# Kernel tuning notes

Hardware: AMD Instinct MI355X
Metric: run time of the kernel (lower is better)

The kernel has to match this reference:

```python
import jax, jax.numpy as jnp
import numpy as np

N = 50000   # nodes per node type
D = 256     # in_dim == out_dim
H = 8       # num heads
DK = D // H # 32
E = 500000  # edges per edge type
LN_EPS = 1e-5


def setup_inputs() -> dict:
    key = jax.random.key(0)
    ks = jax.random.split(key, 16)
    w = lambda k, shape: jax.random.normal(k, shape, dtype=jnp.float32) * 0.05
    xav = np.sqrt(6.0 / (DK + DK))
    return {
        'feats': jax.random.normal(ks[0], (2, N, D), dtype=jnp.float32),
        'Wk': w(ks[1], (2, D, D)), 'bk': jnp.zeros((2, D), jnp.float32),
        'Wq': w(ks[2], (2, D, D)), 'bq': jnp.zeros((2, D), jnp.float32),
        'Wv': w(ks[3], (2, D, D)), 'bv': jnp.zeros((2, D), jnp.float32),
        'Wa': w(ks[4], (2, D, D)), 'ba': jnp.zeros((2, D), jnp.float32),
        'ln_w': jnp.ones((2, D), jnp.float32), 'ln_b': jnp.zeros((2, D), jnp.float32),
        'skip': jnp.ones((2,), jnp.float32),
        'mu': jnp.ones((2, H), jnp.float32),
        'w_att': jax.random.uniform(ks[5], (2, H, DK, DK), jnp.float32, -xav, xav),
        'w_msg': jax.random.uniform(ks[6], (2, H, DK, DK), jnp.float32, -xav, xav),
        'src': jax.random.randint(ks[7], (2, E), 0, N, dtype=jnp.int32),
        'dst': jax.random.randint(ks[8], (2, E), 0, N, dtype=jnp.int32),
    }


def _edge_softmax(scores, seg, n):
    # scores: (E, H); softmax over edges sharing the same destination node
    m = jax.ops.segment_max(scores, seg, num_segments=n)          # (N, H)
    e = jnp.exp(scores - m[seg])
    s = jax.ops.segment_sum(e, seg, num_segments=n)               # (N, H)
    return e / s[seg]


def _forward(feats, Wk, bk, Wq, bq, Wv, bv, Wa, ba, ln_w, ln_b, skip,
             mu, w_att, w_msg, src, dst):
    # canonical etypes: 0 = author->paper, 1 = paper->author
    stypes, dtypes = (0, 1), (1, 0)
    scale = 1.0 / jnp.sqrt(jnp.asarray(DK, feats.dtype))
    h = [None, None]
    for et in range(2):
        st, dt = stypes[et], dtypes[et]
        s_idx, d_idx = src[et], dst[et]
        k = (feats[st] @ Wk[st] + bk[st]).reshape(N, H, DK)
        k = jnp.einsum('nhi,hij->nhj', k, w_att[et])
        v = (feats[st] @ Wv[st] + bv[st]).reshape(N, H, DK)
        v = jnp.einsum('nhi,hij->nhj', v, w_msg[et])
        q = (feats[dt] @ Wq[dt] + bq[dt]).reshape(N, H, DK)
        t = jnp.einsum('ehd,ehd->eh', q[d_idx], k[s_idx])         # (E, H)
        attn = _edge_softmax(t * mu[et] * scale, d_idx, N)        # (E, H)
        msg = v[s_idx] * attn[..., None]                          # (E, H, DK)
        h[dt] = jax.ops.segment_sum(msg, d_idx, num_segments=N).reshape(N, D)
    h = jnp.stack(h)  # (2, N, D); each ntype receives from exactly one etype

    trans = jnp.einsum('tnd,tde->tne', h, Wa) + ba[:, None, :]
    alpha = jax.nn.sigmoid(skip)[:, None, None]
    out = alpha * trans + (1.0 - alpha) * feats
    mean = out.mean(-1, keepdims=True)
    var = out.var(-1, keepdims=True)
    out = (out - mean) * jax.lax.rsqrt(var + LN_EPS)
    return out * ln_w[:, None, :] + ln_b[:, None, :]


def reference(feats, Wk, bk, Wq, bq, Wv, bv, Wa, ba, ln_w, ln_b, skip,
              mu, w_att, w_msg, src, dst):
    return _forward(feats, Wk, bk, Wq, bq, Wv, bv, Wa, ba, ln_w, ln_b, skip,
                    mu, w_att, w_msg, src, dst)
```

## Files before the change

### kernel.cpp

```cpp
#include <hip/hip_runtime.h>
#include <hip/hip_bf16.h>

#define D 256
#define H 8
#define DK 32

typedef unsigned short ushort_t;
typedef unsigned int uint_t;
typedef __attribute__((ext_vector_type(4))) float floatx4;
typedef __attribute__((ext_vector_type(2))) float floatx2;
typedef __attribute__((ext_vector_type(8))) short shortx8;
typedef __attribute__((ext_vector_type(8))) unsigned short ushortx8;

typedef __attribute__((address_space(3))) void lds_void_t;
typedef const __attribute__((address_space(1))) void gbl_void_t;

__device__ __forceinline__ float b2f(ushort_t u) {
    return __uint_as_float(((uint_t)u) << 16);
}
__device__ __forceinline__ floatx2 b2x2(uint_t u) {
    floatx2 r;
    r.x = __uint_as_float(u << 16);
    r.y = __uint_as_float(u & 0xffff0000u);
    return r;
}
__device__ __forceinline__ ushort_t f2b(float f) {
    uint_t u = __float_as_uint(f);
    uint_t r = (u + 0x7FFFu + ((u >> 16) & 1u)) >> 16;
    return (ushort_t)r;
}
__device__ __forceinline__ void async_cp16(const void* g, void* l) {
    __builtin_amdgcn_global_load_lds((gbl_void_t*)g, (lds_void_t*)l, 16, 0, 0);
}

__global__ void cvt_bf16(const float* __restrict__ in, ushort_t* __restrict__ out, size_t n4) {
    size_t i = (size_t)blockIdx.x * blockDim.x + threadIdx.x;
    if (i >= n4) return;
    float4 v = ((const float4*)in)[i];
    ushort4 o;
    o.x = f2b(v.x); o.y = f2b(v.y); o.z = f2b(v.z); o.w = f2b(v.w);
    ((ushort4*)out)[i] = o;
}

__global__ void zero_int(int* __restrict__ p, int n) {
    int i = blockIdx.x * blockDim.x + threadIdx.x;
    if (i < n) p[i] = 0;
}

__global__ void fold_weights(const float* __restrict__ Wk, const float* __restrict__ bk,
                             const float* __restrict__ Wv, const float* __restrict__ bv,
                             const float* __restrict__ w_att, const float* __restrict__ w_msg,
                             float* __restrict__ Wkc, float* __restrict__ bkc,
                             float* __restrict__ Wvc, float* __restrict__ bvc) {
    int r = blockIdx.x, et = blockIdx.y, which = blockIdx.z;
    int tid = threadIdx.x;
    const float* Wsrc = (which ? Wv : Wk) + (size_t)et * D * D + (size_t)r * D;
    const float* wt   = (which ? w_msg : w_att) + (size_t)et * H * DK * DK;
    float* Wdst = (which ? Wvc : Wkc) + (size_t)et * D * D;
    __shared__ float wrow[D];
    wrow[tid] = Wsrc[tid];
    __syncthreads();
    int h = tid >> 5, j = tid & 31;
    const float* wth = wt + h * DK * DK;
    float acc = 0.f;
#pragma unroll 8
    for (int i = 0; i < DK; i++) acc += wrow[h * 32 + i] * wth[i * 32 + j];
    Wdst[(size_t)r * D + tid] = acc;
    if (r == 0) {
        const float* bsrc = (which ? bv : bk) + et * D;
        float* bdst = (which ? bvc : bkc) + et * D;
        float bacc = 0.f;
#pragma unroll 8
        for (int i = 0; i < DK; i++) bacc += bsrc[h * 32 + i] * wth[i * 32 + j];
        bdst[tid] = bacc;
    }
}

__global__ void pack_weights(const float* __restrict__ Wq, const float* __restrict__ bq,
                             const float* __restrict__ Wkc, const float* __restrict__ bkc,
                             const float* __restrict__ Wvc, const float* __restrict__ bvc,
                             const float* __restrict__ Wa,
                             ushort_t* __restrict__ WT_all, ushort_t* __restrict__ WaT,
                             float* __restrict__ bias_all) {
    int idx = blockIdx.x * blockDim.x + threadIdx.x;
    const int NW = 2 * 768 * 256;
    if (idx < NW) {
        int t = idx / (768 * 256);
        int rem = idx - t * 768 * 256;
        int n = rem >> 8, k = rem & 255;
        int sec = n >> 8, nn = n & 255;
        const float* W = (sec == 0) ? Wq : (sec == 1) ? Wkc : Wvc;
        WT_all[idx] = f2b(W[(size_t)t * D * D + (size_t)k * D + nn]);
    } else if (idx < NW + 2 * 256 * 256) {
        int r = idx - NW;
        int t = r / (256 * 256);
        int rem = r - t * 256 * 256;
        int n = rem >> 8, k = rem & 255;
        WaT[r] = f2b(Wa[(size_t)t * D * D + (size_t)k * D + n]);
    }
    if (idx < 2 * 768) {
        int t = idx / 768, n = idx % 768;
        int sec = n >> 8, nn = n & 255;
        const float* b = (sec == 0) ? bq : (sec == 1) ? bkc : bvc;
        bias_all[idx] = b[t * D + nn];
    }
}

#define TM 128
#define TN 128
#define TKK 32
__launch_bounds__(256)
__global__ void gemm_mfma(const ushort_t* __restrict__ A0, int lda, size_t aStr,
                          const ushort_t* __restrict__ BT0, size_t bStr,
                          const float* __restrict__ bias0, int biasStr,
                          ushort_t* __restrict__ C0, int ldc, size_t cStr,
                          int cShift, int M) {
    __shared__ ushort_t As[2][TM * TKK];
    __shared__ ushort_t Bs[2][TN * TKK];
    int tid = threadIdx.x;
    int w = tid >> 6, lane = tid & 63;
    int t = blockIdx.z;
    const ushort_t* A  = A0 + (size_t)t * aStr;
    const ushort_t* BT = BT0 + (size_t)t * bStr;
    const float* bias  = bias0 + (size_t)t * biasStr;
    ushort_t* C        = C0 + (size_t)t * cStr;

    int nwg  = gridDim.x * gridDim.y;
    int orig = blockIdx.y * gridDim.x + blockIdx.x;
    int q = nwg >> 3, r = nwg & 7;
    int xcd = orig & 7, loc = orig >> 3;
    int wgid = (xcd < r ? xcd * (q + 1) : r * (q + 1) + (xcd - r) * q) + loc;
    int ncol = gridDim.y;
    int rowt = wgid / ncol;
    int colt = wgid - rowt * ncol;
    int bm = rowt * TM;
    int bn = colt * TN;

    int wm = (w & 1) * 64, wn = (w >> 1) * 64;

    floatx4 acc[4][4] = {};

    int srow = lane >> 2;
    int scol = (lane & 3) * 8;
    int fr = lane & 15, fq = lane >> 4;

#define GEMM_STAGE(b, kc)                                                     \
    {                                                                         \
        _Pragma("unroll")                                                     \
        for (int j = 0; j < 2; j++) {                                         \
            int rr = w * 32 + j * 16;                                         \
            int gr = bm + rr + srow; if (gr >= M) gr = M - 1;                 \
            async_cp16(A + (size_t)gr * lda + (kc) + scol, As[b] + rr * TKK); \
            int gn = bn + rr + srow;                                          \
            async_cp16(BT + (size_t)gn * 256 + (kc) + scol, Bs[b] + rr * TKK);\
        }                                                                     \
    }

    GEMM_STAGE(0, 0);
#pragma unroll
    for (int s = 0; s < 8; s++) {
        int cur = s & 1;
        if (s < 7) {
            GEMM_STAGE(cur ^ 1, (s + 1) * TKK);
            __builtin_amdgcn_s_waitcnt(0x0F74);
        } else {
            __builtin_amdgcn_s_waitcnt(0x0F70);
        }
        __syncthreads();

        shortx8 af[4], bf[4];
#pragma unroll
        for (int i = 0; i < 4; i++)
            af[i] = *(const shortx8*)(As[cur] + (wm + i * 16 + fr) * TKK + fq * 8);
#pragma unroll
        for (int j = 0; j < 4; j++)
            bf[j] = *(const shortx8*)(Bs[cur] + (wn + j * 16 + fr) * TKK + fq * 8);
#pragma unroll
        for (int i = 0; i < 4; i++)
#pragma unroll
            for (int j = 0; j < 4; j++)
                acc[i][j] = __builtin_amdgcn_mfma_f32_16x16x32_bf16(af[i], bf[j], acc[i][j], 0, 0, 0);
        __syncthreads();
    }
#undef GEMM_STAGE

#pragma unroll
    for (int i = 0; i < 4; i++) {
#pragma unroll
        for (int j = 0; j < 4; j++) {
            int col = bn + wn + j * 16 + fr;
            float bv = bias[col];
#pragma unroll
            for (int rr = 0; rr < 4; rr++) {
                int row = bm + wm + i * 16 + fq * 4 + rr;
                if (row < M) C[(size_t)row * ldc + cShift + col] = f2b(acc[i][j][rr] + bv);
            }
        }
    }
}

__global__ void count_deg(const int* __restrict__ dst, int* __restrict__ deg,
                          int N, int E) {
    int i = blockIdx.x * blockDim.x + threadIdx.x;
    if (i >= 2 * E) return;
    int et = i / E, e = i - et * E;
    int d = dst[(size_t)et * E + e];
    atomicAdd(&deg[(1 - et) * N + d], 1);
}

__launch_bounds__(256)
__global__ void scan_blocks(int* __restrict__ deg, int* __restrict__ bsum, int n) {
    __shared__ int wsum[4];
    int tid = threadIdx.x, lane = tid & 63, w = tid >> 6;
    int i = blockIdx.x * 256 + tid;
    int v = (i < n) ? deg[i] : 0;
    int x = v;
#pragma unroll
    for (int off = 1; off < 64; off <<= 1) {
        int y = __shfl_up(x, off);
        if (lane >= off) x += y;
    }
    if (lane == 63) wsum[w] = x;
    __syncthreads();
    int add = 0;
    if (w > 0) add += wsum[0];
    if (w > 1) add += wsum[1];
    if (w > 2) add += wsum[2];
    int incl = x + add;
    if (i < n) deg[i] = incl - v;
    if (tid == 255) bsum[blockIdx.x] = incl;
}

__launch_bounds__(512)
__global__ void scan_tops(int* __restrict__ bsum, int* __restrict__ row_ptr,
                          int nb, int n) {
    __shared__ int wsum[8];
    int tid = threadIdx.x, lane = tid & 63, w = tid >> 6;
    int v = (tid < nb) ? bsum[tid] : 0;
    int x = v;
#pragma unroll
    for (int off = 1; off < 64; off <<= 1) {
        int y = __shfl_up(x, off);
        if (lane >= off) x += y;
    }
    if (lane == 63) wsum[w] = x;
    __syncthreads();
    int add = 0;
    for (int j = 0; j < w; j++) add += wsum[j];
    int incl = x + add;
    if (tid < nb) bsum[tid] = incl - v;
    if (tid == nb - 1) row_ptr[n] = incl;
}

__launch_bounds__(256)
__global__ void scan_apply(const int* __restrict__ excl, const int* __restrict__ bsum,
                           int* __restrict__ row_ptr, int* __restrict__ cursor, int n) {
    int i = blockIdx.x * 256 + threadIdx.x;
    if (i >= n) return;
    int e = excl[i] + bsum[blockIdx.x];
    row_ptr[i] = e;
    cursor[i] = e;
}

__global__ void fill_edges(const int* __restrict__ src, const int* __restrict__ dst,
                           int* __restrict__ cursor, int* __restrict__ ebuf,
                           int N, int E) {
    int i = blockIdx.x * blockDim.x + threadIdx.x;
    if (i >= 2 * E) return;
    int et = i / E, e = i - et * E;
    int d = dst[(size_t)et * E + e];
    int s = src[(size_t)et * E + e];
    int pos = atomicAdd(&cursor[(1 - et) * N + d], 1);
    ebuf[pos] = s;
}

__launch_bounds__(256)
__global__ void node_aggregate(ushort_t* __restrict__ QKV, const float* __restrict__ mu,
                               const int* __restrict__ row_ptr, const int* __restrict__ ebuf,
                               int N) {
    int wid = (blockIdx.x * blockDim.x + threadIdx.x) >> 6;
    int lane = threadIdx.x & 63;
    if (wid >= 2 * N) return;
    int dt = (wid >= N) ? 1 : 0;
    int et = 1 - dt;
    int l = lane & 31;
    int half = lane >> 5;
    int h = l >> 2;

    uint4 qu = ((const uint4*)(QKV + (size_t)wid * 768))[l];
    floatx2 q01 = b2x2(qu.x), q23 = b2x2(qu.y), q45 = b2x2(qu.z), q67 = b2x2(qu.w);
    float sc = mu[et * H + h] * 0.17677669529663687f;
    int beg = row_ptr[wid], end = row_ptr[wid + 1];
    const ushort_t* KVb = QKV + (size_t)et * N * 768 + l * 8;

    floatx2 a01 = {0.f, 0.f}, a23 = {0.f, 0.f}, a45 = {0.f, 0.f}, a67 = {0.f, 0.f};
    float ssum = 0.f;

#define AGG_COMPUTE(kk, vv)                                              \
    {                                                                    \
        floatx2 pv = q01 * b2x2(kk.x);                                   \
        pv += q23 * b2x2(kk.y);                                          \
        pv += q45 * b2x2(kk.z);                                          \
        pv += q67 * b2x2(kk.w);                                          \
        float pp = pv.x + pv.y;                                          \
        pp += __shfl_xor(pp, 1);                                         \
        pp += __shfl_xor(pp, 2);                                         \
        float ex = __expf(pp * sc);                                      \
        ssum += ex;                                                      \
        floatx2 e2 = {ex, ex};                                           \
        a01 += e2 * b2x2(vv.x);                                          \
        a23 += e2 * b2x2(vv.y);                                          \
        a45 += e2 * b2x2(vv.z);                                          \
        a67 += e2 * b2x2(vv.w);                                          \
    }

    int p = beg + half;
    uint4 kA = {}, vA = {}, kB = {}, vB = {};
    int sC = 0, sD = 0;
    if (p < end) {
        int sA = ebuf[p];
        const ushort_t* r0 = KVb + (size_t)sA * 768;
        kA = *(const uint4*)(r0 + 256);
        vA = *(const uint4*)(r0 + 512);
        sC = (p + 4 < end) ? ebuf[p + 4] : sA;
    }
    if (p + 2 < end) {
        int sB = ebuf[p + 2];
        const ushort_t* r1 = KVb + (size_t)sB * 768;
        kB = *(const uint4*)(r1 + 256);
        vB = *(const uint4*)(r1 + 512);
        sD = (p + 6 < end) ? ebuf[p + 6] : sB;
    }
    while (p < end) {
        uint4 nk = kA, nv = vA;
        int sE = sC;
        if (p + 4 < end) {
            const ushort_t* rr = KVb + (size_t)sC * 768;
            nk = *(const uint4*)(rr + 256);
            nv = *(const uint4*)(rr + 512);
            if (p + 8 < end) sE = ebuf[p + 8];
        }
        AGG_COMPUTE(kA, vA);
        kA = nk; vA = nv; sC = sE;
        p += 2;
        if (p >= end) break;
        nk = kB; nv = vB; sE = sD;
        if (p + 4 < end) {
            const ushort_t* rr = KVb + (size_t)sD * 768;
            nk = *(const uint4*)(rr + 256);
            nv = *(const uint4*)(rr + 512);
            if (p + 8 < end) sE = ebuf[p + 8];
        }
        AGG_COMPUTE(kB, vB);
        kB = nk; vB = nv; sD = sE;
        p += 2;
    }
#undef AGG_COMPUTE

    ssum += __shfl_xor(ssum, 32);
    a01.x += __shfl_xor(a01.x, 32); a01.y += __shfl_xor(a01.y, 32);
    a23.x += __shfl_xor(a23.x, 32); a23.y += __shfl_xor(a23.y, 32);
    a45.x += __shfl_xor(a45.x, 32); a45.y += __shfl_xor(a45.y, 32);
    a67.x += __shfl_xor(a67.x, 32); a67.y += __shfl_xor(a67.y, 32);
    float r = (ssum > 0.f) ? 1.0f / ssum : 0.0f;
    if (half == 0) {
        ushortx8 hv;
        hv[0] = f2b(a01.x * r); hv[1] = f2b(a01.y * r);
        hv[2] = f2b(a23.x * r); hv[3] = f2b(a23.y * r);
        hv[4] = f2b(a45.x * r); hv[5] = f2b(a45.y * r);
        hv[6] = f2b(a67.x * r); hv[7] = f2b(a67.y * r);
        ((ushortx8*)(QKV + (size_t)wid * 768))[l] = hv;
    }
}

__launch_bounds__(256)
__global__ void skip_ln(const ushort_t* __restrict__ trans, const ushort_t* __restrict__ featsb,
                        const float* __restrict__ lnw, const float* __restrict__ lnb,
                        const float* __restrict__ skip, float* __restrict__ out, int N) {
    int wid = (blockIdx.x * blockDim.x + threadIdx.x) >> 6;
    int lane = threadIdx.x & 63;
    if (wid >= 2 * N) return;
    int t = (wid >= N) ? 1 : 0;
    float alpha = 1.0f / (1.0f + __expf(-skip[t]));
    float beta = 1.0f - alpha;
    ushort4 tu = ((const ushort4*)(trans + (size_t)wid * 768))[lane];
    ushort4 fu = ((const ushort4*)(featsb + (size_t)wid * D))[lane];
    float x0 = alpha * b2f(tu.x) + beta * b2f(fu.x);
    float x1 = alpha * b2f(tu.y) + beta * b2f(fu.y);
    float x2 = alpha * b2f(tu.z) + beta * b2f(fu.z);
    float x3 = alpha * b2f(tu.w) + beta * b2f(fu.w);
    float s  = x0 + x1 + x2 + x3;
    float sq = x0 * x0 + x1 * x1 + x2 * x2 + x3 * x3;
#pragma unroll
    for (int off = 1; off < 64; off <<= 1) {
        s  += __shfl_xor(s,  off);
        sq += __shfl_xor(sq, off);
    }
    float mean = s * (1.0f / 256.0f);
    float var  = sq * (1.0f / 256.0f) - mean * mean;
    float r = rsqrtf(var + 1e-5f);
    float4 w4 = ((const float4*)(lnw + t * D))[lane];
    float4 b4 = ((const float4*)(lnb + t * D))[lane];
    float4 o;
    o.x = (x0 - mean) * r * w4.x + b4.x;
    o.y = (x1 - mean) * r * w4.y + b4.y;
    o.z = (x2 - mean) * r * w4.z + b4.z;
    o.w = (x3 - mean) * r * w4.w + b4.w;
    ((float4*)(out + (size_t)wid * D))[lane] = o;
}

extern "C" void kernel_launch(void* const* d_in, const int* in_sizes, int n_in,
                              void* d_out, int out_size, void* d_ws, size_t ws_size,
                              hipStream_t stream) {
    const float* feats = (const float*)d_in[0];
    const float* Wk    = (const float*)d_in[1];
    const float* bk    = (const float*)d_in[2];
    const float* Wq    = (const float*)d_in[3];
    const float* bq    = (const float*)d_in[4];
    const float* Wv    = (const float*)d_in[5];
    const float* bv    = (const float*)d_in[6];
    const float* Wa    = (const float*)d_in[7];
    const float* ba    = (const float*)d_in[8];
    const float* ln_w  = (const float*)d_in[9];
    const float* ln_b  = (const float*)d_in[10];
    const float* skip  = (const float*)d_in[11];
    const float* mu    = (const float*)d_in[12];
    const float* w_att = (const float*)d_in[13];
    const float* w_msg = (const float*)d_in[14];
    const int*   src   = (const int*)d_in[15];
    const int*   dst   = (const int*)d_in[16];
    float* out = (float*)d_out;

    const int N = in_sizes[0] / (2 * D);
    const int E = in_sizes[15] / 2;
    const int NN = 2 * N;
    const size_t ND2 = 2 * (size_t)N * D;

    float* ws = (float*)d_ws;
    size_t off = 0;
    float* Wkc  = ws + off; off += 2 * (size_t)D * D;
    float* Wvc  = ws + off; off += 2 * (size_t)D * D;
    float* bkc  = ws + off; off += 2 * D;
    float* bvc  = ws + off; off += 2 * D;
    float* bias_all = ws + off; off += 2 * 768;
    ushort_t* WT_all = (ushort_t*)(ws + off); off += 2 * 768 * 256 / 2;
    ushort_t* WaT    = (ushort_t*)(ws + off); off += 2 * 256 * 256 / 2;
    ushort_t* featsb = (ushort_t*)(ws + off); off += ND2 / 2;
    ushort_t* QKV    = (ushort_t*)(ws + off); off += 2 * (size_t)N * 768 / 2;
    int* deg     = (int*)(ws + off); off += NN;
    int* row_ptr = (int*)(ws + off); off += NN + 1;
    int* cursor  = (int*)(ws + off); off += NN + 1;
    int* ebuf    = (int*)(ws + off); off += 2 * (size_t)E;
    int* bsum    = (int*)(ws + off); off += 512;

    const int nb = (NN + 255) / 256;

    zero_int<<<(NN + 255) / 256, 256, 0, stream>>>(deg, NN);
    count_deg<<<(2 * E + 255) / 256, 256, 0, stream>>>(dst, deg, N, E);
    scan_blocks<<<nb, 256, 0, stream>>>(deg, bsum, NN);
    scan_tops<<<1, 512, 0, stream>>>(bsum, row_ptr, nb, NN);
    scan_apply<<<nb, 256, 0, stream>>>(deg, bsum, row_ptr, cursor, NN);
    fill_edges<<<(2 * E + 255) / 256, 256, 0, stream>>>(src, dst, cursor, ebuf, N, E);

    fold_weights<<<dim3(D, 2, 2), 256, 0, stream>>>(Wk, bk, Wv, bv, w_att, w_msg,
                                                    Wkc, bkc, Wvc, bvc);
    pack_weights<<<(2 * 768 * 256 + 2 * 256 * 256 + 255) / 256, 256, 0, stream>>>(
        Wq, bq, Wkc, bkc, Wvc, bvc, Wa, WT_all, WaT, bias_all);

    cvt_bf16<<<(unsigned)((ND2 / 4 + 255) / 256), 256, 0, stream>>>(feats, featsb, ND2 / 4);

    dim3 qkv_grid((N + TM - 1) / TM, 768 / TN, 2);
    gemm_mfma<<<qkv_grid, 256, 0, stream>>>(featsb, D, (size_t)N * D,
                                            WT_all, (size_t)768 * 256,
                                            bias_all, 768,
                                            QKV, 768, (size_t)N * 768, 0, N);

    node_aggregate<<<(NN * 64 + 255) / 256, 256, 0, stream>>>(QKV, mu, row_ptr, ebuf, N);

    dim3 tr_grid((N + TM - 1) / TM, 256 / TN, 2);
    gemm_mfma<<<tr_grid, 256, 0, stream>>>(QKV, 768, (size_t)N * 768,
                                           WaT, (size_t)256 * 256,
                                           ba, 256,
                                           QKV, 768, (size_t)N * 768, 256, N);

    skip_ln<<<(NN * 64 + 255) / 256, 256, 0, stream>>>(QKV + 256, featsb,
                                                       ln_w, ln_b, skip, out, N);
}
```

Measured before the change: 603.5 us.

## Fuse Wa projection GEMM with skip blend and LayerNorm epilogue

Replaces the separate Wa GEMM and skip_ln kernel with one kernel. Each block computes a 64-row by full-256-column output tile, then does the sigmoid skip blend, the row mean/variance reduction (via shuffles and LDS) and the LayerNorm in registers, writing fp32 output directly. This removes the bf16 round trip of the trans intermediate and one launch. In exchange, the epilogue uses narrower, less coalesced loads of featsb and stores of out, and each block reloads the whole Wa tile. The node aggregation is also split into two launches, one per node type.

Measured after the change: 620.5 us. 1.03x slower.

```diff
diff --git a/kernel.cpp b/kernel.cpp
--- a/kernel.cpp
+++ b/kernel.cpp
@@ -113,8 +113,7 @@
 __global__ void gemm_mfma(const ushort_t* __restrict__ A0, int lda, size_t aStr,
                           const ushort_t* __restrict__ BT0, size_t bStr,
                           const float* __restrict__ bias0, int biasStr,
-                          ushort_t* __restrict__ C0, int ldc, size_t cStr,
-                          int cShift, int M) {
+                          ushort_t* __restrict__ C0, int ldc, size_t cStr, int M) {
     __shared__ ushort_t As[2][TM * TKK];
     __shared__ ushort_t Bs[2][TN * TKK];
     int tid = threadIdx.x;
@@ -193,8 +192,127 @@
 #pragma unroll
             for (int rr = 0; rr < 4; rr++) {
                 int row = bm + wm + i * 16 + fq * 4 + rr;
-                if (row < M) C[(size_t)row * ldc + cShift + col] = f2b(acc[i][j][rr] + bv);
+                if (row < M) C[(size_t)row * ldc + col] = f2b(acc[i][j][rr] + bv);
             }
+        }
+    }
+}
+
+#define TM2 64
+__launch_bounds__(256)
+__global__ void gemm_trans_ln(const ushort_t* __restrict__ QKV,
+                              const ushort_t* __restrict__ featsb,
+                              const ushort_t* __restrict__ WaT,
+                              const float* __restrict__ ba,
+                              const float* __restrict__ lnw, const float* __restrict__ lnb,
+                              const float* __restrict__ skip,
+                              float* __restrict__ out, int N) {
+    __shared__ ushort_t As[2][TM2 * TKK];
+    __shared__ ushort_t Bs[2][256 * TKK];
+    __shared__ float red_s[4][TM2], red_q[4][TM2];
+    int tid = threadIdx.x;
+    int w = tid >> 6, lane = tid & 63;
+    int t = blockIdx.z;
+    const ushort_t* A  = QKV + (size_t)t * N * 768;
+    const ushort_t* BT = WaT + (size_t)t * 256 * 256;
+    int bm = blockIdx.x * TM2;
+    int wn = w * 64;
+
+    floatx4 acc[4][4] = {};
+
+    int srow = lane >> 2;
+    int scol = (lane & 3) * 8;
+    int fr = lane & 15, fq = lane >> 4;
+
+#define TRANS_STAGE(b, kc)                                                      \
+    {                                                                           \
+        int ar = w * 16;                                                        \
+        int gr = bm + ar + srow; if (gr >= N) gr = N - 1;                       \
+        async_cp16(A + (size_t)gr * 768 + (kc) + scol, As[b] + ar * TKK);       \
+        _Pragma("unroll")                                                       \
+        for (int j = 0; j < 4; j++) {                                           \
+            int br = w * 64 + j * 16;                                           \
+            async_cp16(BT + (size_t)(br + srow) * 256 + (kc) + scol,            \
+                       Bs[b] + br * TKK);                                       \
+        }                                                                       \
+    }
+
+    TRANS_STAGE(0, 0);
+#pragma unroll
+    for (int s = 0; s < 8; s++) {
+        int cur = s & 1;
+        if (s < 7) {
+            TRANS_STAGE(cur ^ 1, (s + 1) * TKK);
+            __builtin_amdgcn_s_waitcnt(0x0F75);
+        } else {
+            __builtin_amdgcn_s_waitcnt(0x0F70);
+        }
+        __syncthreads();
+
+        shortx8 af[4], bf[4];
+#pragma unroll
+        for (int i = 0; i < 4; i++)
+            af[i] = *(const shortx8*)(As[cur] + (i * 16 + fr) * TKK + fq * 8);
+#pragma unroll
+        for (int j = 0; j < 4; j++)
+            bf[j] = *(const shortx8*)(Bs[cur] + (wn + j * 16 + fr) * TKK + fq * 8);
+#pragma unroll
+        for (int i = 0; i < 4; i++)
+#pragma unroll
+            for (int j = 0; j < 4; j++)
+                acc[i][j] = __builtin_amdgcn_mfma_f32_16x16x32_bf16(af[i], bf[j], acc[i][j], 0, 0, 0);
+        __syncthreads();
+    }
+#undef TRANS_STAGE
+
+    float alpha = 1.0f / (1.0f + __expf(-skip[t]));
+    float beta = 1.0f - alpha;
+    float bav[4], lw[4], lb[4];
+#pragma unroll
+    for (int j = 0; j < 4; j++) {
+        int col = wn + j * 16 + fr;
+        bav[j] = ba[t * 256 + col];
+        lw[j]  = lnw[t * 256 + col];
+        lb[j]  = lnb[t * 256 + col];
+    }
+#pragma unroll
+    for (int i = 0; i < 4; i++) {
+#pragma unroll
+        for (int rr = 0; rr < 4; rr++) {
+            int row = i * 16 + fq * 4 + rr;
+            int grow = bm + row; if (grow >= N) grow = N - 1;
+            const ushort_t* frow = featsb + ((size_t)t * N + grow) * 256;
+            float s = 0.f, sq = 0.f;
+#pragma unroll
+            for (int j = 0; j < 4; j++) {
+                float x = alpha * (acc[i][j][rr] + bav[j]) + beta * b2f(frow[wn + j * 16 + fr]);
+                acc[i][j][rr] = x;
+                s += x; sq += x * x;
+            }
+#pragma unroll
+            for (int off = 1; off < 16; off <<= 1) {
+                s  += __shfl_xor(s,  off);
+                sq += __shfl_xor(sq, off);
+            }
+            if (fr == 0) { red_s[w][row] = s; red_q[w][row] = sq; }
+        }
+    }
+    __syncthreads();
+#pragma unroll
+    for (int i = 0; i < 4; i++) {
+#pragma unroll
+        for (int rr = 0; rr < 4; rr++) {
+            int row = i * 16 + fq * 4 + rr;
+            if (bm + row >= N) continue;
+            float s  = red_s[0][row] + red_s[1][row] + red_s[2][row] + red_s[3][row];
+            float sq = red_q[0][row] + red_q[1][row] + red_q[2][row] + red_q[3][row];
+            float mean = s * (1.0f / 256.0f);
+            float var  = sq * (1.0f / 256.0f) - mean * mean;
+            float rinv = rsqrtf(var + 1e-5f);
+            float* orow = out + ((size_t)t * N + bm + row) * 256;
+#pragma unroll
+            for (int j = 0; j < 4; j++)
+                orow[wn + j * 16 + fr] = (acc[i][j][rr] - mean) * rinv * lw[j] + lb[j];
         }
     }
 }
@@ -277,10 +395,10 @@
 __launch_bounds__(256)
 __global__ void node_aggregate(ushort_t* __restrict__ QKV, const float* __restrict__ mu,
                                const int* __restrict__ row_ptr, const int* __restrict__ ebuf,
-                               int N) {
-    int wid = (blockIdx.x * blockDim.x + threadIdx.x) >> 6;
+                               int N, int wbase) {
+    int wid = ((blockIdx.x * blockDim.x + threadIdx.x) >> 6) + wbase;
     int lane = threadIdx.x & 63;
-    if (wid >= 2 * N) return;
+    if (wid >= wbase + N) return;
     int dt = (wid >= N) ? 1 : 0;
     int et = 1 - dt;
     int l = lane & 31;
@@ -371,42 +489,6 @@
         hv[6] = f2b(a67.x * r); hv[7] = f2b(a67.y * r);
         ((ushortx8*)(QKV + (size_t)wid * 768))[l] = hv;
     }
-}
-
-__launch_bounds__(256)
-__global__ void skip_ln(const ushort_t* __restrict__ trans, const ushort_t* __restrict__ featsb,
-                        const float* __restrict__ lnw, const float* __restrict__ lnb,
-                        const float* __restrict__ skip, float* __restrict__ out, int N) {
-    int wid = (blockIdx.x * blockDim.x + threadIdx.x) >> 6;
-    int lane = threadIdx.x & 63;
-    if (wid >= 2 * N) return;
-    int t = (wid >= N) ? 1 : 0;
-    float alpha = 1.0f / (1.0f + __expf(-skip[t]));
-    float beta = 1.0f - alpha;
-    ushort4 tu = ((const ushort4*)(trans + (size_t)wid * 768))[lane];
-    ushort4 fu = ((const ushort4*)(featsb + (size_t)wid * D))[lane];
-    float x0 = alpha * b2f(tu.x) + beta * b2f(fu.x);
-    float x1 = alpha * b2f(tu.y) + beta * b2f(fu.y);
-    float x2 = alpha * b2f(tu.z) + beta * b2f(fu.z);
-    float x3 = alpha * b2f(tu.w) + beta * b2f(fu.w);
-    float s  = x0 + x1 + x2 + x3;
-    float sq = x0 * x0 + x1 * x1 + x2 * x2 + x3 * x3;
-#pragma unroll
-    for (int off = 1; off < 64; off <<= 1) {
-        s  += __shfl_xor(s,  off);
-        sq += __shfl_xor(sq, off);
-    }
-    float mean = s * (1.0f / 256.0f);
-    float var  = sq * (1.0f / 256.0f) - mean * mean;
-    float r = rsqrtf(var + 1e-5f);
-    float4 w4 = ((const float4*)(lnw + t * D))[lane];
-    float4 b4 = ((const float4*)(lnb + t * D))[lane];
-    float4 o;
-    o.x = (x0 - mean) * r * w4.x + b4.x;
-    o.y = (x1 - mean) * r * w4.y + b4.y;
-    o.z = (x2 - mean) * r * w4.z + b4.z;
-    o.w = (x3 - mean) * r * w4.w + b4.w;
-    ((float4*)(out + (size_t)wid * D))[lane] = o;
 }
 
 extern "C" void kernel_launch(void* const* d_in, const int* in_sizes, int n_in,
@@ -473,16 +555,12 @@
     gemm_mfma<<<qkv_grid, 256, 0, stream>>>(featsb, D, (size_t)N * D,
                                             WT_all, (size_t)768 * 256,
                                             bias_all, 768,
-                                            QKV, 768, (size_t)N * 768, 0, N);
-
-    node_aggregate<<<(NN * 64 + 255) / 256, 256, 0, stream>>>(QKV, mu, row_ptr, ebuf, N);
-
-    dim3 tr_grid((N + TM - 1) / TM, 256 / TN, 2);
-    gemm_mfma<<<tr_grid, 256, 0, stream>>>(QKV, 768, (size_t)N * 768,
-                                           WaT, (size_t)256 * 256,
-                                           ba, 256,
-                                           QKV, 768, (size_t)N * 768, 256, N);
-
-    skip_ln<<<(NN * 64 + 255) / 256, 256, 0, stream>>>(QKV + 256, featsb,
-                                                       ln_w, ln_b, skip, out, N);
-}
+                                            QKV, 768, (size_t)N * 768, N);
+
+    node_aggregate<<<((size_t)N * 64 + 255) / 256, 256, 0, stream>>>(QKV, mu, row_ptr, ebuf, N, 0);
+    node_aggregate<<<((size_t)N * 64 + 255) / 256, 256, 0, stream>>>(QKV, mu, row_ptr, ebuf, N, N);
+
+    dim3 tr_grid((N + TM2 - 1) / TM2, 1, 2);
+    gemm_trans_ln<<<tr_grid, 256, 0, stream>>>(QKV, featsb, WaT, ba,
+                                               ln_w, ln_b, skip, out, N);
+}
```
